# Kernel optimization log

Measured on AMD Instinct MI355X. Metric: run time of the kernel, lower is better.

Reference implementation:

```python
import jax, jax.numpy as jnp
import numpy as np

NUM_USERS = 100000
NUM_ITEMS = 200000
N_NODES = NUM_USERS + NUM_ITEMS
LATENT_DIM = 64
N_LAYERS = 3
NNZ = 4000000


def setup_inputs() -> dict:
    key = jax.random.key(0)
    k1, k2, k3, k4, k5 = jax.random.split(key, 5)
    user_emb = 0.1 * jax.random.normal(k1, (NUM_USERS, LATENT_DIM), dtype=jnp.float32)
    item_emb = 0.1 * jax.random.normal(k2, (NUM_ITEMS, LATENT_DIM), dtype=jnp.float32)
    edge_rows = jax.random.randint(k3, (NNZ,), 0, N_NODES, dtype=jnp.int32)
    edge_cols = jax.random.randint(k4, (NNZ,), 0, N_NODES, dtype=jnp.int32)
    # normalized adjacency values (positive, small, like 1/sqrt(d_i d_j))
    edge_vals = jax.random.uniform(k5, (NNZ,), dtype=jnp.float32) * 0.1
    return {"user_emb": user_emb, "item_emb": item_emb,
            "edge_rows": edge_rows, "edge_cols": edge_cols, "edge_vals": edge_vals}


def _spmm(edge_rows, edge_cols, edge_vals, x, n):
    # sparse (COO) @ dense: gather source rows, scale, scatter-add to dest rows
    msg = edge_vals[:, None] * x[edge_cols]          # [nnz, D]
    return jax.ops.segment_sum(msg, edge_rows, num_segments=n)


def reference(user_emb, item_emb, edge_rows, edge_cols, edge_vals):
    n_users = user_emb.shape[0]
    n = n_users + item_emb.shape[0]
    all_emb = jnp.concatenate([user_emb, item_emb], axis=0)  # [N, D]
    embs = [all_emb]
    for _ in range(N_LAYERS):
        all_emb = _spmm(edge_rows, edge_cols, edge_vals, all_emb, n)
        embs.append(all_emb)
    light_out = jnp.mean(jnp.stack(embs, axis=1), axis=1)   # [N, D]
    users = light_out[:n_users]
    items = light_out[n_users:]
    return users, items
```

## Files before the change

kernel.cpp:

```cpp
#include <hip/hip_runtime.h>


#define N_USERS  100000
#define N_ITEMS  200000
#define N_NODES_ 300000
#define DIM      64
#define NNZ_     4000000
#define BSHIFT   10
#define NBUCKET  ((N_NODES_ + 1023) >> 10)
#define BCAP     14336
#define PA_CHUNK 4096
#define PA_BLOCKS ((NNZ_ + PA_CHUNK - 1) / PA_CHUNK)

__device__ __forceinline__ unsigned short f2bf(float f) {
    unsigned u = __float_as_uint(f);
    unsigned r = 0x7fffu + ((u >> 16) & 1u);
    return (unsigned short)((u + r) >> 16);
}
__device__ __forceinline__ void fma8(float* acc, float v, uint4 r) {
    acc[0] = fmaf(v, __uint_as_float(r.x << 16), acc[0]);
    acc[1] = fmaf(v, __uint_as_float(r.x & 0xffff0000u), acc[1]);
    acc[2] = fmaf(v, __uint_as_float(r.y << 16), acc[2]);
    acc[3] = fmaf(v, __uint_as_float(r.y & 0xffff0000u), acc[3]);
    acc[4] = fmaf(v, __uint_as_float(r.z << 16), acc[4]);
    acc[5] = fmaf(v, __uint_as_float(r.z & 0xffff0000u), acc[5]);
    acc[6] = fmaf(v, __uint_as_float(r.w << 16), acc[6]);
    acc[7] = fmaf(v, __uint_as_float(r.w & 0xffff0000u), acc[7]);
}
__device__ __forceinline__ uint4 pack8(const float* f) {
    unsigned a = (unsigned)f2bf(f[0]) | ((unsigned)f2bf(f[1]) << 16);
    unsigned b = (unsigned)f2bf(f[2]) | ((unsigned)f2bf(f[3]) << 16);
    unsigned c = (unsigned)f2bf(f[4]) | ((unsigned)f2bf(f[5]) << 16);
    unsigned d = (unsigned)f2bf(f[6]) | ((unsigned)f2bf(f[7]) << 16);
    return make_uint4(a, b, c, d);
}
__device__ __forceinline__ void unpack8(float* f, uint4 r) {
    f[0] = __uint_as_float(r.x << 16); f[1] = __uint_as_float(r.x & 0xffff0000u);
    f[2] = __uint_as_float(r.y << 16); f[3] = __uint_as_float(r.y & 0xffff0000u);
    f[4] = __uint_as_float(r.z << 16); f[5] = __uint_as_float(r.z & 0xffff0000u);
    f[6] = __uint_as_float(r.w << 16); f[7] = __uint_as_float(r.w & 0xffff0000u);
}

__global__ void init_bf(const float4* __restrict__ u, const float4* __restrict__ it,
                        uint4* __restrict__ Abf) {
    const int n_u = N_USERS * DIM / 8;
    const int n_t = N_NODES_ * DIM / 8;
    int i = blockIdx.x * blockDim.x + threadIdx.x;
    if (i >= n_t) return;
    float4 a, b;
    if (i < n_u) { a = u[2 * i];           b = u[2 * i + 1]; }
    else         { int j = i - n_u; a = it[2 * j]; b = it[2 * j + 1]; }
    float f[8] = {a.x, a.y, a.z, a.w, b.x, b.y, b.z, b.w};
    Abf[i] = pack8(f);
}

__global__ void gcur_init2(int* __restrict__ gcursor) {
    int t = threadIdx.x;
    if (t < NBUCKET) gcursor[t] = t * BCAP;
}

__global__ __launch_bounds__(256) void passA(const int* __restrict__ rows,
                                             const int* __restrict__ cols,
                                             const float* __restrict__ vals,
                                             int* __restrict__ gcursor,
                                             int2* __restrict__ binned) {
    __shared__ int  hist[NBUCKET];
    __shared__ int  base_l[NBUCKET];
    __shared__ int  gshift[NBUCKET];
    __shared__ int  sc[256];
    __shared__ int2 stage[PA_CHUNK];
    __shared__ unsigned short bIdA[PA_CHUNK];

    int tid = threadIdx.x;
    int base = blockIdx.x * PA_CHUNK;
    int cnt = NNZ_ - base; if (cnt > PA_CHUNK) cnt = PA_CHUNK;

    for (int i = tid; i < NBUCKET; i += 256) hist[i] = 0;
    __syncthreads();

    int rr[16], cc[16], vv[16];
    #pragma unroll
    for (int k = 0; k < 16; ++k) {
        int i = tid + (k << 8);
        if (i < cnt) {
            int e = base + i;
            rr[k] = rows[e];
            cc[k] = cols[e];
            vv[k] = __float_as_int(vals[e]);
            atomicAdd(&hist[rr[k] >> BSHIFT], 1);
        } else rr[k] = -1;
    }
    __syncthreads();

    int i0 = 2 * tid, i1 = 2 * tid + 1;
    int c0 = (i0 < NBUCKET) ? hist[i0] : 0;
    int c1 = (i1 < NBUCKET) ? hist[i1] : 0;
    sc[tid] = c0 + c1;
    __syncthreads();
    for (int off = 1; off < 256; off <<= 1) {
        int t = (tid >= off) ? sc[tid - off] : 0;
        __syncthreads();
        sc[tid] += t;
        __syncthreads();
    }
    int excl = (tid == 0) ? 0 : sc[tid - 1];
    if (i0 < NBUCKET) {
        base_l[i0] = excl;
        int g0 = c0 ? atomicAdd(&gcursor[i0], c0) : 0;
        gshift[i0] = g0 - excl;
        hist[i0] = 0;
    }
    if (i1 < NBUCKET) {
        base_l[i1] = excl + c0;
        int g1 = c1 ? atomicAdd(&gcursor[i1], c1) : 0;
        gshift[i1] = g1 - (excl + c0);
        hist[i1] = 0;
    }
    __syncthreads();

    #pragma unroll
    for (int k = 0; k < 16; ++k) {
        if (rr[k] >= 0) {
            int b = rr[k] >> BSHIFT;
            int kk = atomicAdd(&hist[b], 1);
            int pos = base_l[b] + kk;
            stage[pos] = make_int2(cc[k] | ((rr[k] & 1023) << 19), vv[k]);
            bIdA[pos] = (unsigned short)b;
        }
    }
    __syncthreads();

    #pragma unroll
    for (int k = 0; k < 16; ++k) {
        int i = tid + (k << 8);
        if (i < cnt) binned[gshift[bIdA[i]] + i] = stage[i];
    }
}

__global__ void bucket_scan(const int* __restrict__ gcursor,
                            int* __restrict__ bucket_base,
                            int* __restrict__ row_start) {
    __shared__ int lds[512];
    int t = threadIdx.x;
    int c = (t < NBUCKET) ? (gcursor[t] - t * BCAP) : 0;
    lds[t] = c;
    __syncthreads();
    for (int off = 1; off < 512; off <<= 1) {
        int v = (t >= off) ? lds[t - off] : 0;
        __syncthreads();
        lds[t] += v;
        __syncthreads();
    }
    if (t < NBUCKET) bucket_base[t] = lds[t] - c;
    if (t == 0) row_start[N_NODES_] = NNZ_;
}

__global__ __launch_bounds__(1024) void passB(const int* __restrict__ gcursor,
                                              const int* __restrict__ bucket_base,
                                              const int2* __restrict__ binned,
                                              int* __restrict__ row_start,
                                              int2* __restrict__ sedge) {
    __shared__ int lcnt[1024];
    int b = blockIdx.x;
    int t = threadIdx.x;
    int base = b * BCAP;
    int cnt = gcursor[b] - base;
    int csr0 = bucket_base[b];
    lcnt[t] = 0;
    __syncthreads();

    int lo[14], hv[14];
    #pragma unroll
    for (int k = 0; k < 14; ++k) {
        int i = t + (k << 10);
        if (i < cnt) {
            int2 p = binned[base + i];
            lo[k] = p.x; hv[k] = p.y;
            atomicAdd(&lcnt[((unsigned)p.x >> 19) & 1023], 1);
        } else lo[k] = -1;
    }
    __syncthreads();

    int v = lcnt[t];
    for (int off = 1; off < 1024; off <<= 1) {
        int tv = (t >= off) ? lcnt[t - off] : 0;
        __syncthreads();
        lcnt[t] += tv;
        __syncthreads();
    }
    int excl = lcnt[t] - v;

    int gr = (b << BSHIFT) + t;
    if (gr < N_NODES_) row_start[gr] = csr0 + excl;
    __syncthreads();
    lcnt[t] = excl;
    __syncthreads();

    #pragma unroll
    for (int k = 0; k < 14; ++k) {
        if (lo[k] >= 0) {
            int rl = ((unsigned)lo[k] >> 19) & 1023;
            int pos = atomicAdd(&lcnt[rl], 1);
            sedge[csr0 + pos] = make_int2(lo[k] & 0x7ffff, hv[k]);
        }
    }
}

template<bool FUSE>
__global__ __launch_bounds__(256) void spmm_bf_t(const int* __restrict__ row_start,
                                                 const int2* __restrict__ sedge,
                                                 const uint4* __restrict__ x,
                                                 uint4* __restrict__ y,
                                                 const float4* __restrict__ u,
                                                 const float4* __restrict__ it,
                                                 const uint4* __restrict__ x1,
                                                 const uint4* __restrict__ x2,
                                                 float4* __restrict__ out) {
    int w = blockIdx.x * 4 + (threadIdx.x >> 6);
    if (w >= N_NODES_) return;
    int lane = threadIdx.x & 63;
    int g = lane >> 3;
    int d = lane & 7;
    int s = row_start[w];
    int e = row_start[w + 1];
    float acc[8] = {0.f, 0.f, 0.f, 0.f, 0.f, 0.f, 0.f, 0.f};
    for (int base = s; base < e; base += 64) {
        int n = e - base; if (n > 64) n = 64;
        int ec = 0, ev = 0;
        if (lane < n) { int2 p = sedge[base + lane]; ec = p.x; ev = p.y; }
        int nG = (n + 7) >> 3;
        int j = 0;
        for (; j + 1 < nG; j += 2) {
            int i0 = (j << 3) + g;
            int i1 = i0 + 8;
            int   c0 = __shfl(ec, i0);
            float v0 = __int_as_float(__shfl(ev, i0));
            int   c1 = __shfl(ec, i1);
            float v1 = __int_as_float(__shfl(ev, i1));
            uint4 r0 = x[(size_t)c0 * 8 + d];
            uint4 r1 = x[(size_t)c1 * 8 + d];
            fma8(acc, v0, r0);
            fma8(acc, v1, r1);
        }
        if (j < nG) {
            int i0 = (j << 3) + g;
            int   c0 = __shfl(ec, i0);
            float v0 = __int_as_float(__shfl(ev, i0));
            uint4 r0 = x[(size_t)c0 * 8 + d];
            fma8(acc, v0, r0);
        }
    }
    #pragma unroll
    for (int k = 0; k < 8; ++k) {
        acc[k] += __shfl_xor(acc[k], 8);
        acc[k] += __shfl_xor(acc[k], 16);
        acc[k] += __shfl_xor(acc[k], 32);
    }
    if (lane < 8) {
        if (!FUSE) {
            y[(size_t)w * 8 + d] = pack8(acc);
        } else {
            const float4* src = (w < N_USERS) ? (u + (size_t)w * 16)
                                              : (it + (size_t)(w - N_USERS) * 16);
            float4 a = src[2 * d];
            float4 b2 = src[2 * d + 1];
            float f0[8] = {a.x, a.y, a.z, a.w, b2.x, b2.y, b2.z, b2.w};
            float f1[8], f2[8];
            unpack8(f1, x1[(size_t)w * 8 + d]);
            unpack8(f2, x2[(size_t)w * 8 + d]);
            float o[8];
            #pragma unroll
            for (int k = 0; k < 8; ++k) o[k] = (f0[k] + f1[k] + f2[k] + acc[k]) * 0.25f;
            out[(size_t)w * 16 + 2 * d]     = make_float4(o[0], o[1], o[2], o[3]);
            out[(size_t)w * 16 + 2 * d + 1] = make_float4(o[4], o[5], o[6], o[7]);
        }
    }
}

extern "C" void kernel_launch(void* const* d_in, const int* in_sizes, int n_in,
                              void* d_out, int out_size, void* d_ws, size_t ws_size,
                              hipStream_t stream) {
    const float* user_emb = (const float*)d_in[0];
    const float* item_emb = (const float*)d_in[1];
    const int*   rows     = (const int*)d_in[2];
    const int*   cols     = (const int*)d_in[3];
    const float* vals     = (const float*)d_in[4];
    float* out = (float*)d_out;

    const size_t nE = (size_t)N_NODES_ * DIM;
    unsigned short* Abf = (unsigned short*)d_ws;
    unsigned short* Bbf = Abf + nE;
    unsigned short* Cbf = Bbf + nE;
    int* row_start   = (int*)(Cbf + nE);
    int* gcursor     = row_start + (N_NODES_ + 2);
    int* bucket_base = gcursor + 512;
    int2* binned = (int2*)(bucket_base + 512);
    int2* sedge  = binned + (size_t)NBUCKET * BCAP;

    const int n_t8 = (int)(nE / 8);
    const int ew_grid   = (n_t8 + 255) / 256;
    const int spmm_grid = (N_NODES_ + 3) / 4;

    gcur_init2<<<1, 512, 0, stream>>>(gcursor);
    passA<<<PA_BLOCKS, 256, 0, stream>>>(rows, cols, vals, gcursor, binned);
    bucket_scan<<<1, 512, 0, stream>>>(gcursor, bucket_base, row_start);
    passB<<<NBUCKET, 1024, 0, stream>>>(gcursor, bucket_base, binned, row_start, sedge);

    init_bf<<<ew_grid, 256, 0, stream>>>((const float4*)user_emb, (const float4*)item_emb,
                                         (uint4*)Abf);
    spmm_bf_t<false><<<spmm_grid, 256, 0, stream>>>(row_start, sedge, (const uint4*)Abf,
                                                    (uint4*)Bbf, nullptr, nullptr,
                                                    nullptr, nullptr, nullptr);
    spmm_bf_t<false><<<spmm_grid, 256, 0, stream>>>(row_start, sedge, (const uint4*)Bbf,
                                                    (uint4*)Cbf, nullptr, nullptr,
                                                    nullptr, nullptr, nullptr);
    spmm_bf_t<true><<<spmm_grid, 256, 0, stream>>>(row_start, sedge, (const uint4*)Cbf,
                                                   nullptr,
                                                   (const float4*)user_emb,
                                                   (const float4*)item_emb,
                                                   (const uint4*)Bbf, (const uint4*)Cbf,
                                                   (float4*)out);
}
```

Measured before the change: 600.3 us.

## Assign one 8-lane group per row in SpMM instead of one wavefront per row

The SpMM kernel changes from one 64-lane wavefront per destination row, which split edges across 8 groups and needed a cross-group shuffle reduction, to one 8-thread group per row, so each wavefront handles 8 rows and each group walks its own edge list serially. This removes the shuffle reduction, the shuffle broadcast of edge data and the lanes left idle on rows with few edges (average degree is about 13). The trade-off is that each group now runs a longer serial loop, with less memory-level parallelism per row and load imbalance between rows in the same wavefront. The grid is now exactly N/32 blocks with no bounds check, which relies on 300000 being divisible by 32.

Result: faster. 553.7 us (-7.8%).

```diff
diff --git a/kernel.cpp b/kernel.cpp
--- a/kernel.cpp
+++ b/kernel.cpp
@@ -216,64 +216,41 @@
                                                  const uint4* __restrict__ x1,
                                                  const uint4* __restrict__ x2,
                                                  float4* __restrict__ out) {
-    int w = blockIdx.x * 4 + (threadIdx.x >> 6);
-    if (w >= N_NODES_) return;
-    int lane = threadIdx.x & 63;
-    int g = lane >> 3;
-    int d = lane & 7;
+    int w = blockIdx.x * 32 + (threadIdx.x >> 3);
+    int d = threadIdx.x & 7;
     int s = row_start[w];
     int e = row_start[w + 1];
     float acc[8] = {0.f, 0.f, 0.f, 0.f, 0.f, 0.f, 0.f, 0.f};
-    for (int base = s; base < e; base += 64) {
-        int n = e - base; if (n > 64) n = 64;
-        int ec = 0, ev = 0;
-        if (lane < n) { int2 p = sedge[base + lane]; ec = p.x; ev = p.y; }
-        int nG = (n + 7) >> 3;
-        int j = 0;
-        for (; j + 1 < nG; j += 2) {
-            int i0 = (j << 3) + g;
-            int i1 = i0 + 8;
-            int   c0 = __shfl(ec, i0);
-            float v0 = __int_as_float(__shfl(ev, i0));
-            int   c1 = __shfl(ec, i1);
-            float v1 = __int_as_float(__shfl(ev, i1));
-            uint4 r0 = x[(size_t)c0 * 8 + d];
-            uint4 r1 = x[(size_t)c1 * 8 + d];
-            fma8(acc, v0, r0);
-            fma8(acc, v1, r1);
-        }
-        if (j < nG) {
-            int i0 = (j << 3) + g;
-            int   c0 = __shfl(ec, i0);
-            float v0 = __int_as_float(__shfl(ev, i0));
-            uint4 r0 = x[(size_t)c0 * 8 + d];
-            fma8(acc, v0, r0);
-        }
-    }
-    #pragma unroll
-    for (int k = 0; k < 8; ++k) {
-        acc[k] += __shfl_xor(acc[k], 8);
-        acc[k] += __shfl_xor(acc[k], 16);
-        acc[k] += __shfl_xor(acc[k], 32);
-    }
-    if (lane < 8) {
-        if (!FUSE) {
-            y[(size_t)w * 8 + d] = pack8(acc);
-        } else {
-            const float4* src = (w < N_USERS) ? (u + (size_t)w * 16)
-                                              : (it + (size_t)(w - N_USERS) * 16);
-            float4 a = src[2 * d];
-            float4 b2 = src[2 * d + 1];
-            float f0[8] = {a.x, a.y, a.z, a.w, b2.x, b2.y, b2.z, b2.w};
-            float f1[8], f2[8];
-            unpack8(f1, x1[(size_t)w * 8 + d]);
-            unpack8(f2, x2[(size_t)w * 8 + d]);
-            float o[8];
-            #pragma unroll
-            for (int k = 0; k < 8; ++k) o[k] = (f0[k] + f1[k] + f2[k] + acc[k]) * 0.25f;
-            out[(size_t)w * 16 + 2 * d]     = make_float4(o[0], o[1], o[2], o[3]);
-            out[(size_t)w * 16 + 2 * d + 1] = make_float4(o[4], o[5], o[6], o[7]);
-        }
+    int i = s;
+    for (; i + 1 < e; i += 2) {
+        int2 p0 = sedge[i];
+        int2 p1 = sedge[i + 1];
+        uint4 r0 = x[((unsigned)p0.x << 3) + d];
+        uint4 r1 = x[((unsigned)p1.x << 3) + d];
+        fma8(acc, __int_as_float(p0.y), r0);
+        fma8(acc, __int_as_float(p1.y), r1);
+    }
+    if (i < e) {
+        int2 p0 = sedge[i];
+        uint4 r0 = x[((unsigned)p0.x << 3) + d];
+        fma8(acc, __int_as_float(p0.y), r0);
+    }
+    if (!FUSE) {
+        y[(size_t)w * 8 + d] = pack8(acc);
+    } else {
+        const float4* src = (w < N_USERS) ? (u + (size_t)w * 16)
+                                          : (it + (size_t)(w - N_USERS) * 16);
+        float4 a  = src[2 * d];
+        float4 b2 = src[2 * d + 1];
+        float f0[8] = {a.x, a.y, a.z, a.w, b2.x, b2.y, b2.z, b2.w};
+        float f1[8], f2[8];
+        unpack8(f1, x1[(size_t)w * 8 + d]);
+        unpack8(f2, x2[(size_t)w * 8 + d]);
+        float o[8];
+        #pragma unroll
+        for (int k = 0; k < 8; ++k) o[k] = (f0[k] + f1[k] + f2[k] + acc[k]) * 0.25f;
+        out[(size_t)w * 16 + 2 * d]     = make_float4(o[0], o[1], o[2], o[3]);
+        out[(size_t)w * 16 + 2 * d + 1] = make_float4(o[4], o[5], o[6], o[7]);
     }
 }
 
@@ -299,7 +276,7 @@
 
     const int n_t8 = (int)(nE / 8);
     const int ew_grid   = (n_t8 + 255) / 256;
-    const int spmm_grid = (N_NODES_ + 3) / 4;
+    const int spmm_grid = N_NODES_ / 32;
 
     gcur_init2<<<1, 512, 0, stream>>>(gcursor);
     passA<<<PA_BLOCKS, 256, 0, stream>>>(rows, cols, vals, gcursor, binned);
```
